# Kernel tuning notes

Hardware: AMD Instinct MI355X
Metric: run time of the kernel (lower is better)

## Reference

```python
import jax, jax.numpy as jnp
import numpy as np

ALPHA = 0.01  # LeakyReLU negative slope
D_OUT = 128   # output_size; a1 is split at this index


def setup_inputs() -> dict:
    key = jax.random.key(0)
    k1, k2, k3, k4 = jax.random.split(key, 4)
    B, N, M, D_IN = 8, 2048, 2048, 256
    input_tensor1 = jax.random.normal(k1, (B, N, D_IN), dtype=jnp.float32)
    input_tensor2 = jax.random.normal(k2, (B, M, D_IN), dtype=jnp.float32)
    attention_mask2 = jnp.zeros((B, 1, M), dtype=jnp.float32)
    # Parameters (xavier-uniform-like scaled normals are fine for a numeric reference)
    W1 = jax.random.normal(k3, (D_IN, D_OUT), dtype=jnp.float32) * (1.414 * np.sqrt(2.0 / (D_IN + D_OUT)))
    a1 = jax.random.normal(k4, (2 * D_OUT, 1), dtype=jnp.float32) * (1.414 * np.sqrt(2.0 / (2 * D_OUT + 1)))
    return {"input_tensor1": input_tensor1, "input_tensor2": input_tensor2,
            "attention_mask2": attention_mask2, "W1": W1, "a1": a1}


def reference(input_tensor1, input_tensor2, attention_mask2, W1, a1):
    # Projections (dropout is identity in eval / p=0)
    Wh1 = jnp.einsum('bnd,de->bne', input_tensor1, W1)  # (B, N, E)
    Wh2 = jnp.einsum('bmd,de->bme', input_tensor2, W1)  # (B, M, E)
    # GAT-style additive score: broadcast outer-sum of two rank-1 projections
    att1 = jnp.einsum('bne,eo->bno', Wh1, a1[:D_OUT, :])   # (B, N, 1)
    att2 = jnp.einsum('bme,eo->bmo', Wh2, a1[D_OUT:, :])   # (B, M, 1)
    e = att1 + jnp.swapaxes(att2, 1, 2)                     # (B, N, M)
    e = jnp.where(e > 0, e, ALPHA * e)                      # LeakyReLU
    scores = e + attention_mask2                            # additive mask
    probs = jax.nn.softmax(scores, axis=-1)                 # (B, N, M)
    context = jnp.einsum('bnm,bme->bne', probs, Wh2)        # (B, N, E)
    return (context, probs)
```

## Files before the change

kernel.cpp:

```cpp
#include <hip/hip_runtime.h>

#define B 8
#define N 2048
#define M 2048
#define DIN 256
#define E 128
#define ALPHA 0.01f
#define LOG2E 1.44269504088896340736f

typedef __attribute__((ext_vector_type(8))) short bf16x8;
typedef __attribute__((ext_vector_type(4))) float f32x4;

#if __has_builtin(__builtin_amdgcn_exp2f)
#define EXP2(x) __builtin_amdgcn_exp2f(x)
#else
#define EXP2(x) exp2f(x)
#endif

__device__ inline ushort f2bf(float x) {
  unsigned u = __float_as_uint(x);
  u = (u + 0x7FFFu + ((u >> 16) & 1u)) >> 16;
  return (ushort)u;
}

__device__ inline float lrelu(float s) { return fmaxf(s, ALPHA * s); }

__device__ inline float getc(const float4& v, int i) {
  return i == 0 ? v.x : i == 1 ? v.y : i == 2 ? v.z : v.w;
}

#define GLDS(gp, lp)                                          \
  __builtin_amdgcn_global_load_lds(                           \
      (const __attribute__((address_space(1))) void*)(gp),    \
      (__attribute__((address_space(3))) void*)(lp), 16, 0, 0)

__global__ __launch_bounds__(256) void prep_v_kernel(
    const float* __restrict__ W1, const float* __restrict__ a1,
    float* __restrict__ v1) {
  int k = threadIdx.x;
  float s1 = 0.f;
#pragma unroll 8
  for (int e = 0; e < E; ++e) s1 += W1[k * E + e] * a1[e];
  v1[k] = s1;
}

__global__ __launch_bounds__(256) void wh2_kernel(
    const float* __restrict__ in2, const float* __restrict__ W1,
    const float* __restrict__ a1, ushort* __restrict__ Wb,
    float* __restrict__ att2) {
  __shared__ float a[32][DIN];
  int r0 = blockIdx.x * 32;
#pragma unroll
  for (int i = 0; i < 8; ++i) {
    int f = (threadIdx.x + i * 256) * 4;
    int r = f >> 8, k = f & 255;
    *(float4*)&a[r][k] = *(const float4*)(in2 + (size_t)(r0 + r) * DIN + k);
  }
  __syncthreads();
  int c  = (threadIdx.x & 31) * 4;
  int tr = (threadIdx.x >> 5) * 4;
  float acc[4][4] = {};
  for (int k4 = 0; k4 < DIN; k4 += 4) {
    float4 av0 = *(const float4*)&a[tr + 0][k4];
    float4 av1 = *(const float4*)&a[tr + 1][k4];
    float4 av2 = *(const float4*)&a[tr + 2][k4];
    float4 av3 = *(const float4*)&a[tr + 3][k4];
#pragma unroll
    for (int kk = 0; kk < 4; ++kk) {
      float4 bv = *(const float4*)(W1 + (size_t)(k4 + kk) * E + c);
      float x0 = getc(av0, kk), x1 = getc(av1, kk);
      float x2 = getc(av2, kk), x3 = getc(av3, kk);
      acc[0][0] += x0 * bv.x; acc[0][1] += x0 * bv.y;
      acc[0][2] += x0 * bv.z; acc[0][3] += x0 * bv.w;
      acc[1][0] += x1 * bv.x; acc[1][1] += x1 * bv.y;
      acc[1][2] += x1 * bv.z; acc[1][3] += x1 * bv.w;
      acc[2][0] += x2 * bv.x; acc[2][1] += x2 * bv.y;
      acc[2][2] += x2 * bv.z; acc[2][3] += x2 * bv.w;
      acc[3][0] += x3 * bv.x; acc[3][1] += x3 * bv.y;
      acc[3][2] += x3 * bv.z; acc[3][3] += x3 * bv.w;
    }
  }
#pragma unroll
  for (int r = 0; r < 4; ++r) {
    int m = r0 + tr + r;
    size_t gbase = (size_t)(m >> 3) * 1024 + (m & 7);
#pragma unroll
    for (int j = 0; j < 4; ++j)
      Wb[gbase + (size_t)(c + j) * 8] = f2bf(acc[r][j]);
  }
  float4 a1b = *(const float4*)(a1 + E + c);
  float p0 = acc[0][0]*a1b.x + acc[0][1]*a1b.y + acc[0][2]*a1b.z + acc[0][3]*a1b.w;
  float p1 = acc[1][0]*a1b.x + acc[1][1]*a1b.y + acc[1][2]*a1b.z + acc[1][3]*a1b.w;
  float p2 = acc[2][0]*a1b.x + acc[2][1]*a1b.y + acc[2][2]*a1b.z + acc[2][3]*a1b.w;
  float p3 = acc[3][0]*a1b.x + acc[3][1]*a1b.y + acc[3][2]*a1b.z + acc[3][3]*a1b.w;
#pragma unroll
  for (int off = 16; off; off >>= 1) {
    p0 += __shfl_xor(p0, off, 32);
    p1 += __shfl_xor(p1, off, 32);
    p2 += __shfl_xor(p2, off, 32);
    p3 += __shfl_xor(p3, off, 32);
  }
  if ((threadIdx.x & 31) == 0) {
    att2[r0 + tr + 0] = p0;
    att2[r0 + tr + 1] = p1;
    att2[r0 + tr + 2] = p2;
    att2[r0 + tr + 3] = p3;
  }
}

__global__ __launch_bounds__(256) void fused_kernel(
    const float* __restrict__ in1, const float* __restrict__ v1,
    const float* __restrict__ att2, const float* __restrict__ mask,
    const ushort* __restrict__ Wb, float* __restrict__ probs,
    float* __restrict__ ctx) {
  __shared__ __align__(16) char smem[49408];
  float* att2s = (float*)smem;
  float* masks = (float*)(smem + 8192);
  char* bufs   = smem + 16384;
  float* rowC  = (float*)(smem + 49152);
  float* rowA  = (float*)(smem + 49280);

  int wg = (blockIdx.x & 7) * 64 + (blockIdx.x >> 3);
  int rt = wg & 63;
  int b  = wg >> 6;
  int row0 = b * N + rt * 32;
  int t0 = threadIdx.x;

  const char* gW = (const char*)(Wb + (size_t)b * M * E);

#define STAGE(bsel, tt)                                        \
  do {                                                         \
    const char* _g = gW + (size_t)(tt) * 16384 + t0 * 16;      \
    char* _l = bufs + (bsel) * 16384 + t0 * 16;                \
    GLDS(_g, _l);                                              \
    GLDS(_g + 4096, _l + 4096);                                \
    GLDS(_g + 8192, _l + 8192);                                \
    GLDS(_g + 12288, _l + 12288);                              \
  } while (0)

  {
    const char* gA = (const char*)(att2 + (size_t)b * M);
    const char* gK = (const char*)(mask + (size_t)b * M);
    char* lA = (char*)att2s;
    char* lK = (char*)masks;
    int so = t0 * 16;
    GLDS(gA + so, lA + so);
    GLDS(gA + so + 4096, lA + so + 4096);
    GLDS(gK + so, lK + so);
    GLDS(gK + so + 4096, lK + so + 4096);
    STAGE(0, 0);
    STAGE(1, 1);
  }
  __syncthreads();

  {
    int srow = t0 >> 3, sub = t0 & 7;
    const float4* x4 = (const float4*)(in1 + (size_t)(row0 + srow) * DIN);
    const float4* v4 = (const float4*)v1;
    float d = 0.f;
#pragma unroll
    for (int i = 0; i < 8; ++i) {
      float4 x = x4[sub + i * 8], vv = v4[sub + i * 8];
      d += x.x * vv.x + x.y * vv.y + x.z * vv.z + x.w * vv.w;
    }
    d += __shfl_xor(d, 1, 8);
    d += __shfl_xor(d, 2, 8);
    d += __shfl_xor(d, 4, 8);
    float sa1 = d;
    const float4* a4 = (const float4*)att2s;
    const float4* k4 = (const float4*)masks;
    float mx = -3.0e38f;
#pragma unroll 4
    for (int i = 0; i < 64; ++i) {
      int idx = sub + i * 8;
      float4 a = a4[idx], k = k4[idx];
      float s0 = lrelu(sa1 + a.x) + k.x;
      float s1 = lrelu(sa1 + a.y) + k.y;
      float s2 = lrelu(sa1 + a.z) + k.z;
      float s3 = lrelu(sa1 + a.w) + k.w;
      mx = fmaxf(mx, fmaxf(fmaxf(s0, s1), fmaxf(s2, s3)));
    }
    mx = fmaxf(mx, __shfl_xor(mx, 1, 8));
    mx = fmaxf(mx, __shfl_xor(mx, 2, 8));
    mx = fmaxf(mx, __shfl_xor(mx, 4, 8));
    float cm = -mx * LOG2E;
    float sum = 0.f;
#pragma unroll 4
    for (int i = 0; i < 64; ++i) {
      int idx = sub + i * 8;
      float4 a = a4[idx], k = k4[idx];
      sum += EXP2(fmaf(lrelu(sa1 + a.x) + k.x, LOG2E, cm));
      sum += EXP2(fmaf(lrelu(sa1 + a.y) + k.y, LOG2E, cm));
      sum += EXP2(fmaf(lrelu(sa1 + a.z) + k.z, LOG2E, cm));
      sum += EXP2(fmaf(lrelu(sa1 + a.w) + k.w, LOG2E, cm));
    }
    sum += __shfl_xor(sum, 1, 8);
    sum += __shfl_xor(sum, 2, 8);
    sum += __shfl_xor(sum, 4, 8);
    if (sub == 0) {
      rowC[srow] = cm - __log2f(sum);
      rowA[srow] = sa1;
    }
  }
  __syncthreads();

  int lane = t0 & 63, w = t0 >> 6;
  int quad = lane >> 4, l16 = lane & 15;
  int m0w = (w & 1) * 16;
  int h   = w >> 1;
  int myrow = row0 + m0w + l16;
  float a1v  = rowA[m0w + l16];
  float crow = rowC[m0w + l16];
  float* prow = probs + (size_t)myrow * M;

  f32x4 acc[8] = {};

  for (int t = 0; t < 32; ++t) {
    const ushort* bw = (const ushort*)(bufs + (t & 1) * 16384);
    int kb = t * 64 + h * 32 + quad * 8;
    float4 a0  = *(const float4*)&att2s[kb];
    float4 a1q = *(const float4*)&att2s[kb + 4];
    float4 k0  = *(const float4*)&masks[kb];
    float4 k1  = *(const float4*)&masks[kb + 4];
    float p0 = EXP2(fmaf(lrelu(a1v + a0.x)  + k0.x, LOG2E, crow));
    float p1 = EXP2(fmaf(lrelu(a1v + a0.y)  + k0.y, LOG2E, crow));
    float p2 = EXP2(fmaf(lrelu(a1v + a0.z)  + k0.z, LOG2E, crow));
    float p3 = EXP2(fmaf(lrelu(a1v + a0.w)  + k0.w, LOG2E, crow));
    float p4 = EXP2(fmaf(lrelu(a1v + a1q.x) + k1.x, LOG2E, crow));
    float p5 = EXP2(fmaf(lrelu(a1v + a1q.y) + k1.y, LOG2E, crow));
    float p6 = EXP2(fmaf(lrelu(a1v + a1q.z) + k1.z, LOG2E, crow));
    float p7 = EXP2(fmaf(lrelu(a1v + a1q.w) + k1.w, LOG2E, crow));
    union { unsigned u[4]; bf16x8 v; } af;
    asm("v_cvt_pk_bf16_f32 %0, %1, %2" : "=v"(af.u[0]) : "v"(p0), "v"(p1));
    asm("v_cvt_pk_bf16_f32 %0, %1, %2" : "=v"(af.u[1]) : "v"(p2), "v"(p3));
    asm("v_cvt_pk_bf16_f32 %0, %1, %2" : "=v"(af.u[2]) : "v"(p4), "v"(p5));
    asm("v_cvt_pk_bf16_f32 %0, %1, %2" : "=v"(af.u[3]) : "v"(p6), "v"(p7));
    f32x4 st0 = {p0, p1, p2, p3};
    f32x4 st1 = {p4, p5, p6, p7};
    __builtin_nontemporal_store(st0, (f32x4*)(prow + kb));
    __builtin_nontemporal_store(st1, (f32x4*)(prow + kb + 4));
    const ushort* bb = bw + (size_t)((h * 4 + quad) * 128) * 8;
#pragma unroll
    for (int cf = 0; cf < 8; ++cf) {
      bf16x8 bfb = *(const bf16x8*)(bb + (size_t)(cf * 16 + l16) * 8);
      acc[cf] =
          __builtin_amdgcn_mfma_f32_16x16x32_bf16(af.v, bfb, acc[cf], 0, 0, 0);
    }
    asm volatile("s_waitcnt vmcnt(2) lgkmcnt(0)" ::: "memory");
    __builtin_amdgcn_s_barrier();
    if (t < 30) STAGE(t & 1, t + 2);
  }
#undef STAGE

  float* red = (float*)bufs;
  if (h == 1) {
    int base = ((w & 1) * 64 + lane) * 36;
#pragma unroll
    for (int cf = 0; cf < 8; ++cf) *(f32x4*)&red[base + cf * 4] = acc[cf];
  }
  __syncthreads();
  if (h == 0) {
    int base = ((w & 1) * 64 + lane) * 36;
#pragma unroll
    for (int cf = 0; cf < 8; ++cf) {
      f32x4 o = *(const f32x4*)&red[base + cf * 4];
      int nn = cf * 16 + l16;
#pragma unroll
      for (int reg = 0; reg < 4; ++reg) {
        int rr = row0 + m0w + quad * 4 + reg;
        ctx[(size_t)rr * E + nn] = acc[cf][reg] + o[reg];
      }
    }
  }
}

extern "C" void kernel_launch(void* const* d_in, const int* in_sizes, int n_in,
                              void* d_out, int out_size, void* d_ws,
                              size_t ws_size, hipStream_t stream) {
  (void)in_sizes; (void)n_in; (void)out_size; (void)ws_size;
  const float* in1  = (const float*)d_in[0];
  const float* in2  = (const float*)d_in[1];
  const float* mask = (const float*)d_in[2];
  const float* W1   = (const float*)d_in[3];
  const float* a1   = (const float*)d_in[4];

  float* ws   = (float*)d_ws;
  float* v1   = ws;
  float* att2 = v1 + DIN;
  ushort* Wb  = (ushort*)(att2 + B * M);

  float* ctx   = (float*)d_out;
  float* probs = ctx + (size_t)B * N * E;

  hipLaunchKernelGGL(prep_v_kernel, dim3(1), dim3(256), 0, stream, W1, a1, v1);
  hipLaunchKernelGGL(wh2_kernel, dim3(B * M / 32), dim3(256), 0, stream,
                     in2, W1, a1, Wb, att2);
  hipLaunchKernelGGL(fused_kernel, dim3(B * N / 32), dim3(256), 0, stream,
                     in1, v1, att2, mask, Wb, probs, ctx);
}
```

Measured before the change: 226.2 us.

## Read Wh2 fragments directly from global, drop LDS double-buffer, fold prep kernel

New measurement: 242.8 us. 1.07x slower.

```diff
diff --git a/kernel.cpp b/kernel.cpp
--- a/kernel.cpp
+++ b/kernel.cpp
@@ -34,20 +34,17 @@
       (const __attribute__((address_space(1))) void*)(gp),    \
       (__attribute__((address_space(3))) void*)(lp), 16, 0, 0)
 
-__global__ __launch_bounds__(256) void prep_v_kernel(
-    const float* __restrict__ W1, const float* __restrict__ a1,
-    float* __restrict__ v1) {
-  int k = threadIdx.x;
-  float s1 = 0.f;
-#pragma unroll 8
-  for (int e = 0; e < E; ++e) s1 += W1[k * E + e] * a1[e];
-  v1[k] = s1;
-}
-
 __global__ __launch_bounds__(256) void wh2_kernel(
     const float* __restrict__ in2, const float* __restrict__ W1,
     const float* __restrict__ a1, ushort* __restrict__ Wb,
-    float* __restrict__ att2) {
+    float* __restrict__ att2, float* __restrict__ v1) {
+  if (blockIdx.x == 0) {
+    int k = threadIdx.x;
+    float s1 = 0.f;
+#pragma unroll 8
+    for (int e = 0; e < E; ++e) s1 += W1[k * E + e] * a1[e];
+    v1[k] = s1;
+  }
   __shared__ float a[32][DIN];
   int r0 = blockIdx.x * 32;
 #pragma unroll
@@ -113,30 +110,17 @@
     const float* __restrict__ att2, const float* __restrict__ mask,
     const ushort* __restrict__ Wb, float* __restrict__ probs,
     float* __restrict__ ctx) {
-  __shared__ __align__(16) char smem[49408];
+  __shared__ __align__(16) char smem[17664];
   float* att2s = (float*)smem;
   float* masks = (float*)(smem + 8192);
-  char* bufs   = smem + 16384;
-  float* rowC  = (float*)(smem + 49152);
-  float* rowA  = (float*)(smem + 49280);
+  float* rowC  = (float*)(smem + 16384);
+  float* rowA  = (float*)(smem + 16512);
 
   int wg = (blockIdx.x & 7) * 64 + (blockIdx.x >> 3);
   int rt = wg & 63;
   int b  = wg >> 6;
   int row0 = b * N + rt * 32;
   int t0 = threadIdx.x;
-
-  const char* gW = (const char*)(Wb + (size_t)b * M * E);
-
-#define STAGE(bsel, tt)                                        \
-  do {                                                         \
-    const char* _g = gW + (size_t)(tt) * 16384 + t0 * 16;      \
-    char* _l = bufs + (bsel) * 16384 + t0 * 16;                \
-    GLDS(_g, _l);                                              \
-    GLDS(_g + 4096, _l + 4096);                                \
-    GLDS(_g + 8192, _l + 8192);                                \
-    GLDS(_g + 12288, _l + 12288);                              \
-  } while (0)
 
   {
     const char* gA = (const char*)(att2 + (size_t)b * M);
@@ -148,8 +132,6 @@
     GLDS(gA + so + 4096, lA + so + 4096);
     GLDS(gK + so, lK + so);
     GLDS(gK + so + 4096, lK + so + 4096);
-    STAGE(0, 0);
-    STAGE(1, 1);
   }
   __syncthreads();
 
@@ -212,11 +194,12 @@
   float a1v  = rowA[m0w + l16];
   float crow = rowC[m0w + l16];
   float* prow = probs + (size_t)myrow * M;
+  const ushort* bbase =
+      Wb + (size_t)b * M * E + (size_t)(h * 4 + quad) * 1024 + (size_t)l16 * 8;
 
   f32x4 acc[8] = {};
 
   for (int t = 0; t < 32; ++t) {
-    const ushort* bw = (const ushort*)(bufs + (t & 1) * 16384);
     int kb = t * 64 + h * 32 + quad * 8;
     float4 a0  = *(const float4*)&att2s[kb];
     float4 a1q = *(const float4*)&att2s[kb + 4];
@@ -239,28 +222,27 @@
     f32x4 st1 = {p4, p5, p6, p7};
     __builtin_nontemporal_store(st0, (f32x4*)(prow + kb));
     __builtin_nontemporal_store(st1, (f32x4*)(prow + kb + 4));
-    const ushort* bb = bw + (size_t)((h * 4 + quad) * 128) * 8;
+    const ushort* bb = bbase + (size_t)t * 8192;
+    __builtin_amdgcn_s_setprio(1);
 #pragma unroll
     for (int cf = 0; cf < 8; ++cf) {
-      bf16x8 bfb = *(const bf16x8*)(bb + (size_t)(cf * 16 + l16) * 8);
+      bf16x8 bfb = *(const bf16x8*)(bb + cf * 128);
       acc[cf] =
           __builtin_amdgcn_mfma_f32_16x16x32_bf16(af.v, bfb, acc[cf], 0, 0, 0);
     }
-    asm volatile("s_waitcnt vmcnt(2) lgkmcnt(0)" ::: "memory");
-    __builtin_amdgcn_s_barrier();
-    if (t < 30) STAGE(t & 1, t + 2);
-  }
-#undef STAGE
-
-  float* red = (float*)bufs;
+    __builtin_amdgcn_s_setprio(0);
+  }
+
+  __syncthreads();
+  float* red = (float*)smem;
   if (h == 1) {
-    int base = ((w & 1) * 64 + lane) * 36;
+    int base = ((w & 1) * 64 + lane) * 34;
 #pragma unroll
     for (int cf = 0; cf < 8; ++cf) *(f32x4*)&red[base + cf * 4] = acc[cf];
   }
   __syncthreads();
   if (h == 0) {
-    int base = ((w & 1) * 64 + lane) * 36;
+    int base = ((w & 1) * 64 + lane) * 34;
 #pragma unroll
     for (int cf = 0; cf < 8; ++cf) {
       f32x4 o = *(const f32x4*)&red[base + cf * 4];
@@ -292,9 +274,8 @@
   float* ctx   = (float*)d_out;
   float* probs = ctx + (size_t)B * N * E;
 
-  hipLaunchKernelGGL(prep_v_kernel, dim3(1), dim3(256), 0, stream, W1, a1, v1);
   hipLaunchKernelGGL(wh2_kernel, dim3(B * M / 32), dim3(256), 0, stream,
-                     in2, W1, a1, Wb, att2);
+                     in2, W1, a1, Wb, att2, v1);
   hipLaunchKernelGGL(fused_kernel, dim3(B * N / 32), dim3(256), 0, stream,
                      in1, v1, att2, mask, Wb, probs, ctx);
 }
```
